# Kernel optimization log

Hardware: AMD Instinct MI355X
Metric: run time of the kernel (lower is better)

Reference implementation:

```python
import jax, jax.numpy as jnp
import numpy as np

N_NODES = 50000
N_EDGES = 640000
N_REL = 8
D_IN = 128
D_HID = 128
D_OUT = 64


def setup_inputs() -> dict:
    key = jax.random.key(0)
    ks = jax.random.split(key, 10)
    x = jax.random.normal(ks[0], (N_NODES, D_IN), dtype=jnp.float32)
    edge_src = jax.random.randint(ks[1], (N_EDGES,), 0, N_NODES, dtype=jnp.int32)
    edge_dst = jax.random.randint(ks[2], (N_EDGES,), 0, N_NODES, dtype=jnp.int32)
    edge_type = jax.random.randint(ks[3], (N_EDGES,), 0, N_REL, dtype=jnp.int32)
    # Glorot-ish scaling for stability
    W1 = jax.random.normal(ks[4], (N_REL, D_IN, D_HID), dtype=jnp.float32) / np.sqrt(D_IN)
    root1 = jax.random.normal(ks[5], (D_IN, D_HID), dtype=jnp.float32) / np.sqrt(D_IN)
    b1 = jnp.zeros((D_HID,), dtype=jnp.float32)
    W2 = jax.random.normal(ks[6], (N_REL, D_HID, D_OUT), dtype=jnp.float32) / np.sqrt(D_HID)
    root2 = jax.random.normal(ks[7], (D_HID, D_OUT), dtype=jnp.float32) / np.sqrt(D_HID)
    b2 = jnp.zeros((D_OUT,), dtype=jnp.float32)
    return {"x": x, "edge_src": edge_src, "edge_dst": edge_dst, "edge_type": edge_type,
            "W1": W1, "root1": root1, "b1": b1, "W2": W2, "root2": root2, "b2": b2}


def rgcn_conv(x, edge_src, edge_dst, edge_type, W, W_root, b):
    """RGCNConv with default per-relation mean aggregation + root weight + bias."""
    N = x.shape[0]
    R, _, O = W.shape
    # Transform all nodes under all relation weights once: [N, R, O]
    xW = jnp.einsum('nd,rdo->nro', x, W)
    # Gather per-edge relation-specific messages: [E, O]
    msg = xW[edge_src, edge_type]
    # Segment per (dst, relation) for mean aggregation
    seg = edge_dst.astype(jnp.int32) * R + edge_type.astype(jnp.int32)
    cnt = jax.ops.segment_sum(jnp.ones_like(edge_type, dtype=x.dtype), seg, num_segments=N * R)
    agg = jax.ops.segment_sum(msg, seg, num_segments=N * R)  # [N*R, O]
    agg = agg / jnp.maximum(cnt, 1.0)[:, None]
    rel_sum = agg.reshape(N, R, O).sum(axis=1)  # [N, O]
    return rel_sum + x @ W_root + b


def reference(x, edge_src, edge_dst, edge_type, W1, root1, b1, W2, root2, b2):
    h = rgcn_conv(x, edge_src, edge_dst, edge_type, W1, root1, b1)
    h = rgcn_conv(h, edge_src, edge_dst, edge_type, W2, root2, b2)
    return jax.nn.sigmoid(h)
```

## Files before the change

### kernel.cpp

```cpp
#include <hip/hip_runtime.h>
#include <math.h>

#define NN 50000
#define NE 640000
#define NR 8
#define SCAN_N (NN * NR)
#define SCAN_CH 2048
#define SCAN_NB ((SCAN_N + SCAN_CH - 1) / SCAN_CH)

typedef __attribute__((ext_vector_type(8))) _Float16 half8;
typedef __attribute__((ext_vector_type(8))) short short8;
typedef __attribute__((ext_vector_type(4))) float f32x4;

__device__ __forceinline__ unsigned short f2h(float f) {
    _Float16 h = (_Float16)f;
    return __builtin_bit_cast(unsigned short, h);
}
__device__ __forceinline__ float h2f(unsigned short u) {
    return (float)__builtin_bit_cast(_Float16, u);
}

__global__ __launch_bounds__(256) void count_kernel(const int* __restrict__ dst,
                                                    const int* __restrict__ typ,
                                                    int* __restrict__ cnt, int E) {
    int e = blockIdx.x * 256 + threadIdx.x;
    if (e < E) atomicAdd(&cnt[dst[e] * NR + typ[e]], 1);
}

__global__ __launch_bounds__(256) void inv_kernel(const int* __restrict__ cnt,
                                                  float* __restrict__ inv, int n) {
    int i = blockIdx.x * 256 + threadIdx.x;
    if (i < n) {
        int c = cnt[i];
        inv[i] = 1.0f / (float)(c > 1 ? c : 1);
    }
}

__global__ __launch_bounds__(256) void scan1_kernel(const int* __restrict__ cnt,
                                                    int* __restrict__ loc,
                                                    int* __restrict__ bsum) {
    __shared__ int s[256];
    const int t = threadIdx.x;
    const int base = blockIdx.x * SCAN_CH + t * 8;
    int v[8];
    int sum = 0;
#pragma unroll
    for (int j = 0; j < 8; ++j) {
        int idx = base + j;
        v[j] = (idx < SCAN_N) ? cnt[idx] : 0;
        sum += v[j];
    }
    s[t] = sum;
    __syncthreads();
    for (int off = 1; off < 256; off <<= 1) {
        int u = (t >= off) ? s[t - off] : 0;
        __syncthreads();
        s[t] += u;
        __syncthreads();
    }
    int run = (t == 0) ? 0 : s[t - 1];
#pragma unroll
    for (int j = 0; j < 8; ++j) {
        int idx = base + j;
        if (idx < SCAN_N) loc[idx] = run;
        run += v[j];
    }
    if (t == 255) bsum[blockIdx.x] = s[255];
}

__global__ __launch_bounds__(256) void scan2_kernel(const int* __restrict__ bsum,
                                                    int* __restrict__ boff, int nb) {
    __shared__ int s[256];
    const int t = threadIdx.x;
    s[t] = (t < nb) ? bsum[t] : 0;
    __syncthreads();
    for (int off = 1; off < 256; off <<= 1) {
        int u = (t >= off) ? s[t - off] : 0;
        __syncthreads();
        s[t] += u;
        __syncthreads();
    }
    if (t < nb) boff[t] = (t == 0) ? 0 : s[t - 1];
    if (t == nb - 1) boff[nb] = s[t];
}

__global__ __launch_bounds__(256) void scan3_kernel(int* __restrict__ rowptr,
                                                    int* __restrict__ start,
                                                    const int* __restrict__ boff, int nb) {
    const int b = blockIdx.x, t = threadIdx.x;
    const int add = boff[b];
#pragma unroll
    for (int j = 0; j < 8; ++j) {
        int idx = b * SCAN_CH + t * 8 + j;
        if (idx < SCAN_N) {
            int v = rowptr[idx] + add;
            rowptr[idx] = v;
            start[idx] = v;
        }
    }
    if (b == 0 && t == 0) rowptr[SCAN_N] = boff[nb];
}

__global__ __launch_bounds__(256) void fill_kernel(const int* __restrict__ src,
                                                   const int* __restrict__ dst,
                                                   const int* __restrict__ typ,
                                                   int* __restrict__ start,
                                                   int* __restrict__ srcrel, int E) {
    int e = blockIdx.x * 256 + threadIdx.x;
    if (e >= E) return;
    int r = typ[e];
    int pos = atomicAdd(&start[dst[e] * NR + r], 1);
    srcrel[pos] = src[e] | (r << 20);
}

__global__ __launch_bounds__(256) void cvt_kernel(const float* __restrict__ x,
                                                  unsigned short* __restrict__ xh, int n4) {
    int i = blockIdx.x * 256 + threadIdx.x;
    if (i >= n4) return;
    float4 v = ((const float4*)x)[i];
    uint2 u;
    u.x = (unsigned)f2h(v.x) | ((unsigned)f2h(v.y) << 16);
    u.y = (unsigned)f2h(v.z) | ((unsigned)f2h(v.w) << 16);
    ((uint2*)xh)[i] = u;
}

__global__ __launch_bounds__(256) void pack_b_kernel(const float* __restrict__ W,
                                                     const float* __restrict__ root,
                                                     unsigned short* __restrict__ Bt, int O) {
    int i = blockIdx.x * 256 + threadIdx.x;
    int NTOT = 9 * O;
    if (i >= NTOT * 128) return;
    int k = i & 127, n = i >> 7;
    float v = (n < 8 * O) ? W[(size_t)(n / O) * 128 * O + (size_t)k * O + (n % O)]
                          : root[(size_t)k * O + (n - 8 * O)];
    Bt[(size_t)n * 128 + k] = f2h(v);
}

#define ACC_EDGE(P, G)                                                        \
    do {                                                                      \
        unsigned r_ = ((unsigned)(P)) >> 20;                                  \
        float vx_ = h2f((unsigned short)((G) & 0xFFFFu));                     \
        float vy_ = h2f((unsigned short)((G) >> 16));                         \
        switch (r_) {                                                         \
            case 0: a0x += vx_; a0y += vy_; break;                            \
            case 1: a1x += vx_; a1y += vy_; break;                            \
            case 2: a2x += vx_; a2y += vy_; break;                            \
            case 3: a3x += vx_; a3y += vy_; break;                            \
            case 4: a4x += vx_; a4y += vy_; break;                            \
            case 5: a5x += vx_; a5y += vy_; break;                            \
            case 6: a6x += vx_; a6y += vy_; break;                            \
            default: a7x += vx_; a7y += vy_; break;                           \
        }                                                                     \
    } while (0)

#define G1(k)                                                                 \
    int p##k = __builtin_amdgcn_readlane(pv, j + k);                          \
    unsigned g##k = X2[(size_t)(p##k & 0xFFFFF) * 64 + lane];

#define A1(k) ACC_EDGE(p##k, g##k)

#define STORE_ROW(R, AX, AY)                                                  \
    do {                                                                      \
        unsigned u_ = (unsigned)f2h((AX) * iv##R) |                           \
                      ((unsigned)f2h((AY) * iv##R) << 16);                    \
        *(unsigned*)(rowp + (((R)*256 + lane * 4) ^ swz)) = u_;               \
    } while (0)

template <int O, bool FINAL>
__global__ __launch_bounds__(512, 6) void fused_layer(
    const int* __restrict__ rp, const int* __restrict__ srcrel,
    const float* __restrict__ inv, const unsigned short* __restrict__ X,
    const unsigned short* __restrict__ Bt, const float* __restrict__ bias,
    void* __restrict__ Hout) {
    __shared__ __align__(16) unsigned short As[16 * 1024];
    __shared__ float pbuf[FINAL ? 4 * 16 * 16 : 4];
    __shared__ int claim_ctr;
    const int t = threadIdx.x;
    const int w = t >> 6, lane = t & 63;
    const int bm = blockIdx.x * 16;
    const unsigned* X2 = (const unsigned*)X;

    if (t == 0) claim_ctr = 0;
    __syncthreads();

    for (;;) {
        int c = 0;
        if (lane == 0) c = atomicAdd(&claim_ctr, 1);
        c = __builtin_amdgcn_readfirstlane(c);
        if (c >= 16) break;
        const int m = c;
        const int d = bm + m;

        float a0x = 0.f, a0y = 0.f, a1x = 0.f, a1y = 0.f;
        float a2x = 0.f, a2y = 0.f, a3x = 0.f, a3y = 0.f;
        float a4x = 0.f, a4y = 0.f, a5x = 0.f, a5y = 0.f;
        float a6x = 0.f, a6y = 0.f, a7x = 0.f, a7y = 0.f;

        const float iv0 = inv[d * 8 + 0], iv1 = inv[d * 8 + 1];
        const float iv2 = inv[d * 8 + 2], iv3 = inv[d * 8 + 3];
        const float iv4 = inv[d * 8 + 4], iv5 = inv[d * 8 + 5];
        const float iv6 = inv[d * 8 + 6], iv7 = inv[d * 8 + 7];

        const int beg = rp[d * 8], end = rp[d * 8 + 8];
        for (int base = beg; base < end; base += 64) {
            int nv = end - base;
            nv = nv > 64 ? 64 : nv;
            int idx = base + (lane < nv ? lane : nv - 1);
            int pv = srcrel[idx];
            int j = 0;
            for (; j + 15 < nv; j += 16) {
                G1(0) G1(1) G1(2) G1(3) G1(4) G1(5) G1(6) G1(7)
                G1(8) G1(9) G1(10) G1(11) G1(12) G1(13) G1(14) G1(15)
                A1(0); A1(1); A1(2); A1(3); A1(4); A1(5); A1(6); A1(7);
                A1(8); A1(9); A1(10); A1(11); A1(12); A1(13); A1(14); A1(15);
            }
            if (j + 7 < nv) {
                G1(0) G1(1) G1(2) G1(3) G1(4) G1(5) G1(6) G1(7)
                A1(0); A1(1); A1(2); A1(3); A1(4); A1(5); A1(6); A1(7);
                j += 8;
            }
            if (j + 3 < nv) {
                G1(0) G1(1) G1(2) G1(3)
                A1(0); A1(1); A1(2); A1(3);
                j += 4;
            }
            for (; j < nv; ++j) {
                int p0 = __builtin_amdgcn_readlane(pv, j);
                unsigned g0 = X2[(size_t)(p0 & 0xFFFFF) * 64 + lane];
                ACC_EDGE(p0, g0);
            }
        }
        char* rowp = (char*)As + m * 2048;
        const int swz = (m & 7) << 4;
        STORE_ROW(0, a0x, a0y);
        STORE_ROW(1, a1x, a1y);
        STORE_ROW(2, a2x, a2y);
        STORE_ROW(3, a3x, a3y);
        STORE_ROW(4, a4x, a4y);
        STORE_ROW(5, a5x, a5y);
        STORE_ROW(6, a6x, a6y);
        STORE_ROW(7, a7x, a7y);
    }
    __syncthreads();

    const int q = lane >> 4, ml = lane & 15;
    int col, ksb;
    if (O == 128) {
        col = w * 16;
        ksb = 0;
    } else {
        col = (w & 3) * 16;
        ksb = (w >> 2) * 18;
    }
    constexpr int NKS = (O == 128) ? 36 : 18;

    f32x4 acc0 = (f32x4)0.f, acc1 = (f32x4)0.f;
    const unsigned short* Xroot = X + (size_t)(bm + ml) * 128;
    const char* arowp = (const char*)As + ml * 2048;
    const int aswz = (ml & 7) << 4;

#pragma unroll 6
    for (int u = 0; u < NKS; ++u) {
        int ks = ksb + u;
        int r = ks >> 2, kk = ks & 3;
        half8 af;
        if (r < 8) {
            af = __builtin_bit_cast(
                half8,
                *(const short8*)(arowp + ((r * 256 + kk * 64 + q * 16) ^ aswz)));
        } else {
            af = __builtin_bit_cast(half8,
                                    *(const short8*)(Xroot + kk * 32 + q * 8));
        }
        half8 bf = __builtin_bit_cast(
            half8,
            *(const short8*)(Bt + (size_t)(r * O + col + ml) * 128 + kk * 32 +
                             q * 8));
        if (u & 1)
            acc1 = __builtin_amdgcn_mfma_f32_16x16x32_f16(af, bf, acc1, 0, 0, 0);
        else
            acc0 = __builtin_amdgcn_mfma_f32_16x16x32_f16(af, bf, acc0, 0, 0, 0);
    }
    f32x4 accv = acc0 + acc1;

    if (!FINAL) {
        float bv = bias[col + ml];
#pragma unroll
        for (int j = 0; j < 4; ++j) {
            int grow = bm + q * 4 + j;
            ((unsigned short*)Hout)[(size_t)grow * O + col + ml] =
                f2h(accv[j] + bv);
        }
    } else {
        const int kg = w >> 2, ci = w & 3;
        if (kg == 1) {
#pragma unroll
            for (int j = 0; j < 4; ++j)
                pbuf[ci * 256 + (q * 4 + j) * 16 + ml] = accv[j];
        }
        __syncthreads();
        if (kg == 0) {
            float bv = bias[col + ml];
#pragma unroll
            for (int j = 0; j < 4; ++j) {
                int grow = bm + q * 4 + j;
                float v = accv[j] + pbuf[ci * 256 + (q * 4 + j) * 16 + ml] + bv;
                ((float*)Hout)[(size_t)grow * O + col + ml] =
                    1.f / (1.f + __expf(-v));
            }
        }
    }
}

extern "C" void kernel_launch(void* const* d_in, const int* in_sizes, int n_in,
                              void* d_out, int out_size, void* d_ws, size_t ws_size,
                              hipStream_t stream) {
    const float* x     = (const float*)d_in[0];
    const int*   esrc  = (const int*)d_in[1];
    const int*   edst  = (const int*)d_in[2];
    const int*   etyp  = (const int*)d_in[3];
    const float* W1    = (const float*)d_in[4];
    const float* root1 = (const float*)d_in[5];
    const float* b1    = (const float*)d_in[6];
    const float* W2    = (const float*)d_in[7];
    const float* root2 = (const float*)d_in[8];
    const float* b2    = (const float*)d_in[9];
    float* out = (float*)d_out;

    char* ws = (char*)d_ws;
    unsigned short* Bt1    = (unsigned short*)ws; ws += (size_t)1152 * 128 * 2;
    unsigned short* Bt2    = (unsigned short*)ws; ws += (size_t)576 * 128 * 2;
    int*            cnt    = (int*)ws;            ws += (size_t)SCAN_N * 4;
    float*          inv    = (float*)ws;          ws += (size_t)SCAN_N * 4;
    int*            rp     = (int*)ws;            ws += (size_t)(SCAN_N + 64) * 4;
    int*            start  = (int*)ws;            ws += (size_t)SCAN_N * 4;
    int*            bsum   = (int*)ws;            ws += (size_t)256 * 4;
    int*            boff   = (int*)ws;            ws += (size_t)257 * 4;
    int*            srcrel = (int*)ws;            ws += (size_t)NE * 4;
    unsigned short* xh     = (unsigned short*)ws; ws += (size_t)NN * 128 * 2;
    unsigned short* h1b    = (unsigned short*)ws;

    hipMemsetAsync(cnt, 0, (size_t)SCAN_N * 4, stream);
    count_kernel<<<(NE + 255) / 256, 256, 0, stream>>>(edst, etyp, cnt, NE);
    inv_kernel<<<(SCAN_N + 255) / 256, 256, 0, stream>>>(cnt, inv, SCAN_N);
    scan1_kernel<<<SCAN_NB, 256, 0, stream>>>(cnt, rp, bsum);
    scan2_kernel<<<1, 256, 0, stream>>>(bsum, boff, SCAN_NB);
    scan3_kernel<<<SCAN_NB, 256, 0, stream>>>(rp, start, boff, SCAN_NB);
    fill_kernel<<<(NE + 255) / 256, 256, 0, stream>>>(esrc, edst, etyp, start, srcrel, NE);

    cvt_kernel<<<(NN * 32 + 255) / 256, 256, 0, stream>>>(x, xh, NN * 32);
    pack_b_kernel<<<(1152 * 128 + 255) / 256, 256, 0, stream>>>(W1, root1, Bt1, 128);
    pack_b_kernel<<<(576 * 128 + 255) / 256, 256, 0, stream>>>(W2, root2, Bt2, 64);

    const int fgrid = NN / 16;

    fused_layer<128, false><<<fgrid, 512, 0, stream>>>(rp, srcrel, inv, xh, Bt1, b1, h1b);
    fused_layer<64, true><<<fgrid, 512, 0, stream>>>(rp, srcrel, inv, h1b, Bt2, b2, out);
}
```

Baseline: 402.6 us.

## Replace switch-based relation accumulate with branchless masked FMAs and simpler edge loop

The per-edge relation switch becomes branchless: each edge does 16 FMAs against all eight accumulators, with the per-relation inverse count as a masked scale, so the final normalisation at store time is dropped. The wave-cooperative index load plus readlane batching of 16/8/4 edges is replaced by per-edge scalar loads unrolled by four. Occupancy hint raised from 6 to 8 waves. This trades divergence-free code for 8x more ALU per edge and less memory-level parallelism in the gather, since only four loads are in flight instead of sixteen.

```diff
diff --git a/kernel.cpp b/kernel.cpp
--- a/kernel.cpp
+++ b/kernel.cpp
@@ -138,36 +138,35 @@
 
 #define ACC_EDGE(P, G)                                                        \
     do {                                                                      \
-        unsigned r_ = ((unsigned)(P)) >> 20;                                  \
+        unsigned rel_ = ((unsigned)(P)) >> 20;                                \
         float vx_ = h2f((unsigned short)((G) & 0xFFFFu));                     \
         float vy_ = h2f((unsigned short)((G) >> 16));                         \
-        switch (r_) {                                                         \
-            case 0: a0x += vx_; a0y += vy_; break;                            \
-            case 1: a1x += vx_; a1y += vy_; break;                            \
-            case 2: a2x += vx_; a2y += vy_; break;                            \
-            case 3: a3x += vx_; a3y += vy_; break;                            \
-            case 4: a4x += vx_; a4y += vy_; break;                            \
-            case 5: a5x += vx_; a5y += vy_; break;                            \
-            case 6: a6x += vx_; a6y += vy_; break;                            \
-            default: a7x += vx_; a7y += vy_; break;                           \
-        }                                                                     \
+        float s0_ = (rel_ == 0) ? iv0 : 0.f;                                  \
+        float s1_ = (rel_ == 1) ? iv1 : 0.f;                                  \
+        float s2_ = (rel_ == 2) ? iv2 : 0.f;                                  \
+        float s3_ = (rel_ == 3) ? iv3 : 0.f;                                  \
+        float s4_ = (rel_ == 4) ? iv4 : 0.f;                                  \
+        float s5_ = (rel_ == 5) ? iv5 : 0.f;                                  \
+        float s6_ = (rel_ == 6) ? iv6 : 0.f;                                  \
+        float s7_ = (rel_ == 7) ? iv7 : 0.f;                                  \
+        a0x = fmaf(vx_, s0_, a0x); a0y = fmaf(vy_, s0_, a0y);                 \
+        a1x = fmaf(vx_, s1_, a1x); a1y = fmaf(vy_, s1_, a1y);                 \
+        a2x = fmaf(vx_, s2_, a2x); a2y = fmaf(vy_, s2_, a2y);                 \
+        a3x = fmaf(vx_, s3_, a3x); a3y = fmaf(vy_, s3_, a3y);                 \
+        a4x = fmaf(vx_, s4_, a4x); a4y = fmaf(vy_, s4_, a4y);                 \
+        a5x = fmaf(vx_, s5_, a5x); a5y = fmaf(vy_, s5_, a5y);                 \
+        a6x = fmaf(vx_, s6_, a6x); a6y = fmaf(vy_, s6_, a6y);                 \
+        a7x = fmaf(vx_, s7_, a7x); a7y = fmaf(vy_, s7_, a7y);                 \
     } while (0)
-
-#define G1(k)                                                                 \
-    int p##k = __builtin_amdgcn_readlane(pv, j + k);                          \
-    unsigned g##k = X2[(size_t)(p##k & 0xFFFFF) * 64 + lane];
-
-#define A1(k) ACC_EDGE(p##k, g##k)
 
 #define STORE_ROW(R, AX, AY)                                                  \
     do {                                                                      \
-        unsigned u_ = (unsigned)f2h((AX) * iv##R) |                           \
-                      ((unsigned)f2h((AY) * iv##R) << 16);                    \
+        unsigned u_ = (unsigned)f2h(AX) | ((unsigned)f2h(AY) << 16);          \
         *(unsigned*)(rowp + (((R)*256 + lane * 4) ^ swz)) = u_;               \
     } while (0)
 
 template <int O, bool FINAL>
-__global__ __launch_bounds__(512, 6) void fused_layer(
+__global__ __launch_bounds__(512, 8) void fused_layer(
     const int* __restrict__ rp, const int* __restrict__ srcrel,
     const float* __restrict__ inv, const unsigned short* __restrict__ X,
     const unsigned short* __restrict__ Bt, const float* __restrict__ bias,
@@ -202,33 +201,25 @@
         const float iv6 = inv[d * 8 + 6], iv7 = inv[d * 8 + 7];
 
         const int beg = rp[d * 8], end = rp[d * 8 + 8];
-        for (int base = beg; base < end; base += 64) {
-            int nv = end - base;
-            nv = nv > 64 ? 64 : nv;
-            int idx = base + (lane < nv ? lane : nv - 1);
-            int pv = srcrel[idx];
-            int j = 0;
-            for (; j + 15 < nv; j += 16) {
-                G1(0) G1(1) G1(2) G1(3) G1(4) G1(5) G1(6) G1(7)
-                G1(8) G1(9) G1(10) G1(11) G1(12) G1(13) G1(14) G1(15)
-                A1(0); A1(1); A1(2); A1(3); A1(4); A1(5); A1(6); A1(7);
-                A1(8); A1(9); A1(10); A1(11); A1(12); A1(13); A1(14); A1(15);
-            }
-            if (j + 7 < nv) {
-                G1(0) G1(1) G1(2) G1(3) G1(4) G1(5) G1(6) G1(7)
-                A1(0); A1(1); A1(2); A1(3); A1(4); A1(5); A1(6); A1(7);
-                j += 8;
-            }
-            if (j + 3 < nv) {
-                G1(0) G1(1) G1(2) G1(3)
-                A1(0); A1(1); A1(2); A1(3);
-                j += 4;
-            }
-            for (; j < nv; ++j) {
-                int p0 = __builtin_amdgcn_readlane(pv, j);
-                unsigned g0 = X2[(size_t)(p0 & 0xFFFFF) * 64 + lane];
-                ACC_EDGE(p0, g0);
-            }
+        int i = beg;
+        for (; i + 3 < end; i += 4) {
+            int p0 = __builtin_amdgcn_readfirstlane(srcrel[i]);
+            int p1 = __builtin_amdgcn_readfirstlane(srcrel[i + 1]);
+            int p2 = __builtin_amdgcn_readfirstlane(srcrel[i + 2]);
+            int p3 = __builtin_amdgcn_readfirstlane(srcrel[i + 3]);
+            unsigned g0 = X2[(size_t)(p0 & 0xFFFFF) * 64 + lane];
+            unsigned g1 = X2[(size_t)(p1 & 0xFFFFF) * 64 + lane];
+            unsigned g2 = X2[(size_t)(p2 & 0xFFFFF) * 64 + lane];
+            unsigned g3 = X2[(size_t)(p3 & 0xFFFFF) * 64 + lane];
+            ACC_EDGE(p0, g0);
+            ACC_EDGE(p1, g1);
+            ACC_EDGE(p2, g2);
+            ACC_EDGE(p3, g3);
+        }
+        for (; i < end; ++i) {
+            int p0 = __builtin_amdgcn_readfirstlane(srcrel[i]);
+            unsigned g0 = X2[(size_t)(p0 & 0xFFFFF) * 64 + lane];
+            ACC_EDGE(p0, g0);
         }
         char* rowp = (char*)As + m * 2048;
         const int swz = (m & 7) << 4;
```

After: 422.4 us. 1.05x slower.
